# Optimization experiments

Hardware: AMD Instinct MI355X
Metric: run time of the kernel (lower is better)

The kernel has to match this reference:

```python
import jax, jax.numpy as jnp
import numpy as np

NUM_HEADS = 16
TOP_K = 32
NEG_INF = -1e9
EPS = 1e-8


def setup_inputs() -> dict:
    key = jax.random.key(0)
    ks = jax.random.split(key, 12)
    B, S, D = 2, 1024, 1024
    M, dk = 8192, D // NUM_HEADS
    w = lambda k: jax.random.normal(k, (D, D), jnp.float32) * 0.02
    return {
        "x": jax.random.normal(ks[0], (B, S, D), jnp.float32),
        "Wq": w(ks[1]), "bq": jnp.zeros((D,), jnp.float32),
        "Wk": w(ks[2]), "bk": jnp.zeros((D,), jnp.float32),
        "Wv": w(ks[3]), "bv": jnp.zeros((D,), jnp.float32),
        "Wo": w(ks[4]), "bo": jnp.zeros((D,), jnp.float32),
        "mem_keys": jax.random.normal(ks[5], (M, dk), jnp.float32),
        "mem_vals": jax.random.normal(ks[6], (M, dk), jnp.float32),
        "gate": jnp.zeros((1,), jnp.float32),
    }


def _normalize(v):
    return v / (jnp.linalg.norm(v, axis=-1, keepdims=True) + EPS)


def reference(x, Wq, bq, Wk, bk, Wv, bv, Wo, bo, mem_keys, mem_vals, gate):
    B, S, D = x.shape
    H = NUM_HEADS
    dk = D // H
    # projections (torch Linear: x @ W.T + b), split heads -> [B,H,S,dk]
    split = lambda t: t.reshape(B, S, H, dk).transpose(0, 2, 1, 3)
    q = split(x @ Wq.T + bq)
    k = split(x @ Wk.T + bk)
    v = split(x @ Wv.T + bv)
    # causal attention
    scores = jnp.einsum("bhqd,bhkd->bhqk", q, k) / jnp.sqrt(jnp.float32(dk))
    causal = jnp.triu(jnp.ones((S, S), bool), k=1)  # True above diagonal
    scores = jnp.where(causal, NEG_INF, scores)
    attn = jax.nn.softmax(scores, axis=-1)
    attn_out = jnp.einsum("bhqk,bhkd->bhqd", attn, v)
    attn_out = attn_out.transpose(0, 2, 1, 3).reshape(B, S, D)
    attn_out = attn_out @ Wo.T + bo
    # KNN memory retrieval on flattened per-head queries [B*H*S, dk]
    flat_q = q.reshape(-1, dk)
    sims = _normalize(flat_q) @ _normalize(mem_keys).T  # [Q, M]
    top_scores, idx = jax.lax.top_k(sims, TOP_K)        # [Q, K]
    gathered = mem_vals[idx]                            # [Q, K, dk]
    memory_out = jnp.sum(gathered * top_scores[..., None], axis=-2)  # [Q, dk]
    memory_out = memory_out.reshape(B, H, S, dk).transpose(0, 2, 1, 3).reshape(B, S, D)
    memory_out = memory_out @ Wo.T + bo
    g = jax.nn.sigmoid(gate)
    return g * memory_out + (1.0 - g) * attn_out
```

## Files before the change

### kernel.cpp

```cpp
#include <hip/hip_runtime.h>
#include <stdint.h>
#include <math.h>

#define BATCH   2
#define SEQ     1024
#define DMODEL  1024
#define NHEADS  16
#define DK      64
#define MKEYS   8192
#define NQ      (BATCH*NHEADS*SEQ)
#define THRC    2.25f
#define KPART   4
#define PKEYS2  (MKEYS/KPART)
#define PCAP    64
#define QCAP2   (KPART*PCAP)

typedef __attribute__((ext_vector_type(8))) short short8;
typedef __attribute__((ext_vector_type(4))) float f32x4;
typedef __attribute__((ext_vector_type(2))) double f64x2;
typedef __attribute__((ext_vector_type(4))) double f64x4;

__device__ __forceinline__ short f2bf(float f) {
  uint32_t u = __builtin_bit_cast(uint32_t, f);
  u = (u + 0x7fffu + ((u >> 16) & 1u)) >> 16;
  return (short)u;
}
__device__ __forceinline__ short8 ld_bf8_f32(const float* p) {
  float4 a = *(const float4*)p; float4 b = *(const float4*)(p + 4);
  short8 r;
  r[0]=f2bf(a.x); r[1]=f2bf(a.y); r[2]=f2bf(a.z); r[3]=f2bf(a.w);
  r[4]=f2bf(b.x); r[5]=f2bf(b.y); r[6]=f2bf(b.z); r[7]=f2bf(b.w);
  return r;
}

__device__ __forceinline__ unsigned long long packP(double v, int id) {
  unsigned long long b = __builtin_bit_cast(unsigned long long, v);
  b = (b & 0x8000000000000000ull) ? ~b : (b | 0x8000000000000000ull);
  return (b & ~0x1FFFull) | (unsigned long long)(8191 - id);
}
__device__ __forceinline__ double unpackV(unsigned long long P) {
  unsigned long long K = P & ~0x1FFFull;
  unsigned long long bits = (K & 0x8000000000000000ull) ? (K ^ 0x8000000000000000ull) : ~K;
  return __builtin_bit_cast(double, bits);
}

__global__ __launch_bounds__(256) void norm_keys(const float* __restrict__ mk,
                                                 double* __restrict__ invn64,
                                                 float* __restrict__ invnf,
                                                 uint16_t* __restrict__ knbf) {
  int wave = threadIdx.x >> 6, lane = threadIdx.x & 63;
  int m = blockIdx.x * 4 + wave;
  double v = (double)mk[(size_t)m * DK + lane];
  double ss = v * v;
  #pragma unroll
  for (int off = 1; off < 64; off <<= 1) ss += __shfl_xor(ss, off);
  double inv = 1.0 / (sqrt(ss) + 1e-8);
  knbf[(size_t)m * DK + lane] = (uint16_t)f2bf((float)(v * inv));
  if (lane == 0) { invn64[m] = inv; invnf[m] = (float)inv; }
}

__device__ __forceinline__ bool probe_decode(const f64x4 d, int base, int mul,
                                             int out[4]) {
  bool ok = true;
  #pragma unroll
  for (int r = 0; r < 4; r++) {
    int v = (int)d[r];
    int t = v - base;
    bool o = ((double)v == d[r]) && (t >= 0) && (t % mul == 0) && ((t / mul) < 16);
    out[r] = t / mul;
    ok = ok && o;
  }
  return ok;
}

__global__ __launch_bounds__(256, 4) void q64_gemm(const float* __restrict__ x,
                                                   const float* __restrict__ Wq,
                                                   const float* __restrict__ bq,
                                                   double* __restrict__ q64q,
                                                   float* __restrict__ qf32,
                                                   uint16_t* __restrict__ qb) {
  __shared__ __align__(16) float Xs[64 * 68];
  __shared__ __align__(16) float Ws[64 * 68];
  int tid = threadIdx.x, lane = tid & 63, w = tid >> 6;
  int bm = blockIdx.y * 64;
  int h = blockIdx.x;

  f64x4 z = {0.0, 0.0, 0.0, 0.0};
  f64x4 d1 = __builtin_amdgcn_mfma_f64_16x16x4f64((double)lane, 1.0, z, 0, 0, 0);
  f64x4 d2 = __builtin_amdgcn_mfma_f64_16x16x4f64(1.0, (double)lane, z, 0, 0, 0);
  int rdec[4], cdec[4];
  bool ok = probe_decode(d1, 96, 4, rdec);
  bool h1A = (bool)__all(ok ? 1 : 0);
  if (!h1A) ok = probe_decode(d1, 6, 16, rdec);
  bool aOK = h1A || (bool)__all(ok ? 1 : 0);
  ok = probe_decode(d2, 96, 4, cdec);
  bool h1B = (bool)__all(ok ? 1 : 0);
  if (!h1B) ok = probe_decode(d2, 6, 16, cdec);
  bool bOK = h1B || (bool)__all(ok ? 1 : 0);
  int iA = h1A ? (lane & 15) : (lane >> 2);
  int kA = h1A ? (lane >> 4) : (lane & 3);
  int jB = h1B ? (lane & 15) : (lane >> 2);
  int kB = h1B ? (lane >> 4) : (lane & 3);
  bool mfma_ok = aOK && bOK;
  if (mfma_ok) {
    f64x4 d3 = __builtin_amdgcn_mfma_f64_16x16x4f64(
        (double)(4 * iA + kA), (double)(jB + 16 * kB), z, 0, 0, 0);
    bool ok3 = true;
    #pragma unroll
    for (int r = 0; r < 4; r++)
      ok3 = ok3 && (d3[r] == (double)(16 * rdec[r] * cdec[r] + 384 * rdec[r] +
                                      6 * cdec[r] + 224));
    mfma_ok = (bool)__all(ok3 ? 1 : 0);
  }

  if (mfma_ok) {
    int wm = (w >> 1) * 32, wn = (w & 1) * 32;
    f64x4 acc[2][2] = {};
    for (int kt = 0; kt < 16; kt++) {
      __syncthreads();
      #pragma unroll
      for (int i = 0; i < 4; i++) {
        int c4 = tid + 256 * i;
        int r = c4 >> 4, q4 = c4 & 15;
        *(float4*)(Xs + r * 68 + q4 * 4) =
            *(const float4*)(x + (size_t)(bm + r) * DMODEL + kt * 64 + q4 * 4);
        *(float4*)(Ws + r * 68 + q4 * 4) =
            *(const float4*)(Wq + (size_t)(h * 64 + r) * DMODEL + kt * 64 + q4 * 4);
      }
      __syncthreads();
      #pragma unroll
      for (int k = 0; k < 64; k += 4) {
        double a0 = (double)Xs[(wm + iA) * 68 + k + kA];
        double a1 = (double)Xs[(wm + 16 + iA) * 68 + k + kA];
        double b0 = (double)Ws[(wn + jB) * 68 + k + kB];
        double b1 = (double)Ws[(wn + 16 + jB) * 68 + k + kB];
        acc[0][0] = __builtin_amdgcn_mfma_f64_16x16x4f64(a0, b0, acc[0][0], 0, 0, 0);
        acc[0][1] = __builtin_amdgcn_mfma_f64_16x16x4f64(a0, b1, acc[0][1], 0, 0, 0);
        acc[1][0] = __builtin_amdgcn_mfma_f64_16x16x4f64(a1, b0, acc[1][0], 0, 0, 0);
        acc[1][1] = __builtin_amdgcn_mfma_f64_16x16x4f64(a1, b1, acc[1][1], 0, 0, 0);
      }
    }
    #pragma unroll
    for (int mi = 0; mi < 2; mi++)
      #pragma unroll
      for (int ni = 0; ni < 2; ni++)
        #pragma unroll
        for (int rg = 0; rg < 4; rg++) {
          int m = bm + wm + mi * 16 + rdec[rg];
          int d = wn + ni * 16 + cdec[rg];
          int b = m >> 10, s = m & 1023;
          size_t qidx = (((size_t)(b * NHEADS + h) * SEQ) + s) * DK + d;
          double val = acc[mi][ni][rg] + (double)bq[h * DK + d];
          q64q[qidx] = val;
          float fv = (float)val;
          qf32[qidx] = fv;
          qb[qidx] = (uint16_t)f2bf(fv);
        }
  } else {
    int tx = tid & 15, ty = tid >> 4;
    double facc[4][4] = {};
    for (int kt = 0; kt < 16; kt++) {
      __syncthreads();
      #pragma unroll
      for (int i = 0; i < 4; i++) {
        int c4 = tid + 256 * i;
        int r = c4 >> 4, q4 = c4 & 15;
        *(float4*)(Xs + r * 68 + q4 * 4) =
            *(const float4*)(x + (size_t)(bm + r) * DMODEL + kt * 64 + q4 * 4);
        *(float4*)(Ws + r * 68 + q4 * 4) =
            *(const float4*)(Wq + (size_t)(h * 64 + r) * DMODEL + kt * 64 + q4 * 4);
      }
      __syncthreads();
      for (int k = 0; k < 64; k++) {
        double bv[4];
        #pragma unroll
        for (int j = 0; j < 4; j++) bv[j] = (double)Ws[(tx + 16 * j) * 68 + k];
        #pragma unroll
        for (int i = 0; i < 4; i++) {
          double a = (double)Xs[(ty * 4 + i) * 68 + k];
          #pragma unroll
          for (int j = 0; j < 4; j++) facc[i][j] = fma(a, bv[j], facc[i][j]);
        }
      }
    }
    #pragma unroll
    for (int i = 0; i < 4; i++)
      #pragma unroll
      for (int j = 0; j < 4; j++) {
        int m = bm + ty * 4 + i, d = tx + 16 * j;
        int b = m >> 10, s = m & 1023;
        size_t qidx = (((size_t)(b * NHEADS + h) * SEQ) + s) * DK + d;
        double val = facc[i][j] + (double)bq[h * DK + d];
        q64q[qidx] = val;
        float fv = (float)val;
        qf32[qidx] = fv;
        qb[qidx] = (uint16_t)f2bf(fv);
      }
  }
}

template<bool AF, bool WF>
__device__ __forceinline__ void gemm_core(const void* __restrict__ Ap,
                                          const void* __restrict__ Wp,
                                          f32x4 acc[4][4], short* As, short* Bs,
                                          int bm, int bn) {
  int tid = threadIdx.x, lane = tid & 63, w = tid >> 6;
  int wm = (w >> 1) * 64, wn = (w & 1) * 64;
  for (int kt = 0; kt < 16; kt++) {
    __syncthreads();
    #pragma unroll
    for (int i = 0; i < 4; i++) {
      int cq = tid + 256 * i;
      int r = cq >> 3, ch = cq & 7;
      size_t aoff = (size_t)(bm + r) * DMODEL + kt * 64 + ch * 8;
      size_t boff = (size_t)(bn + r) * DMODEL + kt * 64 + ch * 8;
      *(short8*)(As + r * 72 + ch * 8) = AF ? ld_bf8_f32((const float*)Ap + aoff)
                                            : *(const short8*)((const uint16_t*)Ap + aoff);
      *(short8*)(Bs + r * 72 + ch * 8) = WF ? ld_bf8_f32((const float*)Wp + boff)
                                            : *(const short8*)((const uint16_t*)Wp + boff);
    }
    __syncthreads();
    #pragma unroll
    for (int kk = 0; kk < 2; kk++) {
      short8 af[4], bfr[4];
      #pragma unroll
      for (int t = 0; t < 4; t++) {
        af[t]  = *(const short8*)(As + (wm + t * 16 + (lane & 15)) * 72 + kk * 32 + (lane >> 4) * 8);
        bfr[t] = *(const short8*)(Bs + (wn + t * 16 + (lane & 15)) * 72 + kk * 32 + (lane >> 4) * 8);
      }
      #pragma unroll
      for (int mi = 0; mi < 4; mi++)
        #pragma unroll
        for (int ni = 0; ni < 4; ni++)
          acc[mi][ni] = __builtin_amdgcn_mfma_f32_16x16x32_bf16(af[mi], bfr[ni], acc[mi][ni], 0, 0, 0);
    }
  }
}

__global__ __launch_bounds__(256) void gemm_kv(
    const float* __restrict__ x,
    const float* __restrict__ Wk, const float* __restrict__ bk,
    const float* __restrict__ Wv, const float* __restrict__ bv,
    uint16_t* __restrict__ kb, uint16_t* __restrict__ vb) {
  __shared__ __align__(16) short As[128 * 72];
  __shared__ __align__(16) short Bs[128 * 72];
  int z = blockIdx.z;
  const float* W    = z == 0 ? Wk : Wv;
  const float* bias = z == 0 ? bk : bv;
  uint16_t* outB    = z == 0 ? kb : vb;
  int bm = blockIdx.y * 128, bn = blockIdx.x * 128;
  f32x4 acc[4][4] = {};
  gemm_core<true, true>(x, W, acc, As, Bs, bm, bn);
  int lane = threadIdx.x & 63, w = threadIdx.x >> 6;
  int wm = (w >> 1) * 64, wn = (w & 1) * 64;
  #pragma unroll
  for (int mi = 0; mi < 4; mi++)
    #pragma unroll
    for (int ni = 0; ni < 4; ni++) {
      int n = bn + wn + ni * 16 + (lane & 15);
      float bvv = bias[n];
      #pragma unroll
      for (int rg = 0; rg < 4; rg++) {
        int m = bm + wm + mi * 16 + (lane >> 4) * 4 + rg;
        float v = acc[mi][ni][rg] + bvv;
        int b = m >> 10, s = m & 1023, h = n >> 6, d = n & 63;
        size_t idx = (((size_t)(b * NHEADS + h) * SEQ) + s) * DK + d;
        outB[idx] = (uint16_t)f2bf(v);
      }
    }
}

__global__ __launch_bounds__(256) void attn_fwd(
    const uint16_t* __restrict__ qb, const uint16_t* __restrict__ kb,
    const uint16_t* __restrict__ vb, float* __restrict__ attnO) {
  __shared__ __align__(16) short Ks[64 * 72];
  __shared__ __align__(16) short Vt[64 * 72];
  __shared__ __align__(16) short Ps[4][16 * 72];
  int tid = threadIdx.x, lane = tid & 63, w = tid >> 6;
  int bx = blockIdx.x;
  int qt = bx & 15, h = (bx >> 4) & 15, b = bx >> 8;
  const uint16_t* Qg = qb + (size_t)(b * NHEADS + h) * SEQ * DK;
  const uint16_t* Kg = kb + (size_t)(b * NHEADS + h) * SEQ * DK;
  const uint16_t* Vg = vb + (size_t)(b * NHEADS + h) * SEQ * DK;
  int qrow0 = qt * 64 + w * 16;
  short8 qfr[2];
  #pragma unroll
  for (int kk = 0; kk < 2; kk++)
    qfr[kk] = *(const short8*)(const void*)(Qg + (size_t)(qrow0 + (lane & 15)) * DK + kk * 32 + (lane >> 4) * 8);
  float m_i[4] = {-1e30f, -1e30f, -1e30f, -1e30f};
  float l_i[4] = {0.f, 0.f, 0.f, 0.f};
  f32x4 Oacc[4] = {};
  for (int kt = 0; kt <= qt; kt++) {
    __syncthreads();
    #pragma unroll
    for (int i = 0; i < 2; i++) {
      int cq = tid + 256 * i;
      int r = cq >> 3, ch = cq & 7;
      short8 g = *(const short8*)(const void*)(Kg + (size_t)(kt * 64 + r) * DK + ch * 8);
      *(short8*)(Ks + r * 72 + ch * 8) = g;
      short8 gv = *(const short8*)(const void*)(Vg + (size_t)(kt * 64 + r) * DK + ch * 8);
      #pragma unroll
      for (int j = 0; j < 8; j++) Vt[(ch * 8 + j) * 72 + r] = gv[j];
    }
    __syncthreads();
    f32x4 sv[4] = {};
    #pragma unroll
    for (int kk = 0; kk < 2; kk++)
      #pragma unroll
      for (int ni = 0; ni < 4; ni++) {
        short8 kf = *(const short8*)(Ks + (ni * 16 + (lane & 15)) * 72 + kk * 32 + (lane >> 4) * 8);
        sv[ni] = __builtin_amdgcn_mfma_f32_16x16x32_bf16(qfr[kk], kf, sv[ni], 0, 0, 0);
      }
    bool diag = (kt == qt);
    #pragma unroll
    for (int ni = 0; ni < 4; ni++)
      #pragma unroll
      for (int rg = 0; rg < 4; rg++) {
        float sc = sv[ni][rg] * 0.125f;
        if (diag) {
          int kcol = kt * 64 + ni * 16 + (lane & 15);
          int qrow = qrow0 + (lane >> 4) * 4 + rg;
          if (kcol > qrow) sc = -1e9f;
        }
        sv[ni][rg] = sc;
      }
    float alpha[4];
    #pragma unroll
    for (int rg = 0; rg < 4; rg++) {
      float v = fmaxf(fmaxf(sv[0][rg], sv[1][rg]), fmaxf(sv[2][rg], sv[3][rg]));
      v = fmaxf(v, __shfl_xor(v, 1)); v = fmaxf(v, __shfl_xor(v, 2));
      v = fmaxf(v, __shfl_xor(v, 4)); v = fmaxf(v, __shfl_xor(v, 8));
      float mn = fmaxf(m_i[rg], v);
      alpha[rg] = expf(m_i[rg] - mn);
      m_i[rg] = mn;
    }
    #pragma unroll
    for (int ni = 0; ni < 4; ni++)
      #pragma unroll
      for (int rg = 0; rg < 4; rg++) sv[ni][rg] = expf(sv[ni][rg] - m_i[rg]);
    #pragma unroll
    for (int rg = 0; rg < 4; rg++) {
      float s = sv[0][rg] + sv[1][rg] + sv[2][rg] + sv[3][rg];
      s += __shfl_xor(s, 1); s += __shfl_xor(s, 2);
      s += __shfl_xor(s, 4); s += __shfl_xor(s, 8);
      l_i[rg] = l_i[rg] * alpha[rg] + s;
    }
    #pragma unroll
    for (int ni = 0; ni < 4; ni++)
      #pragma unroll
      for (int rg = 0; rg < 4; rg++) Oacc[ni][rg] *= alpha[rg];
    short* Pw = &Ps[w][0];
    #pragma unroll
    for (int ni = 0; ni < 4; ni++)
      #pragma unroll
      for (int rg = 0; rg < 4; rg++)
        Pw[((lane >> 4) * 4 + rg) * 72 + ni * 16 + (lane & 15)] = f2bf(sv[ni][rg]);
    #pragma unroll
    for (int kk = 0; kk < 2; kk++) {
      short8 pa = *(const short8*)(Pw + (lane & 15) * 72 + kk * 32 + (lane >> 4) * 8);
      #pragma unroll
      for (int ni = 0; ni < 4; ni++) {
        short8 vf = *(const short8*)(Vt + (ni * 16 + (lane & 15)) * 72 + kk * 32 + (lane >> 4) * 8);
        Oacc[ni] = __builtin_amdgcn_mfma_f32_16x16x32_bf16(pa, vf, Oacc[ni], 0, 0, 0);
      }
    }
  }
  #pragma unroll
  for (int ni = 0; ni < 4; ni++)
    #pragma unroll
    for (int rg = 0; rg < 4; rg++) {
      int row = qrow0 + (lane >> 4) * 4 + rg;
      attnO[((size_t)b * SEQ + row) * DMODEL + h * DK + ni * 16 + (lane & 15)] =
          Oacc[ni][rg] / l_i[rg];
    }
}

__global__ __launch_bounds__(256) void norm_q(const float* __restrict__ qf32,
                                              float* __restrict__ t0arr) {
  int wave = threadIdx.x >> 6, lane = threadIdx.x & 63;
  int q = blockIdx.x * 4 + wave;
  float v = qf32[((size_t)q << 6) + lane];
  float ss = v * v;
  #pragma unroll
  for (int off = 1; off < 64; off <<= 1) ss += __shfl_xor(ss, off);
  if (lane == 0) t0arr[q] = (THRC / 8.0f) * sqrtf(ss);
}

__global__ __launch_bounds__(256) void knn_filter_mfma(
    const uint16_t* __restrict__ qb, const uint16_t* __restrict__ knbf,
    const float* __restrict__ t0arr,
    unsigned short* __restrict__ cand, int* __restrict__ counts) {
  __shared__ __align__(16) short Ks[64 * 68];
  int tid = threadIdx.x, lane = tid & 63, w = tid >> 6;
  int quad = lane >> 4, col = lane & 15;
  int q0 = blockIdx.y * 64;
  int p = blockIdx.x, k0 = p * PKEYS2;
  int qcol = q0 + w * 16 + col;
  short8 aq[2];
  #pragma unroll
  for (int kk = 0; kk < 2; kk++)
    aq[kk] = *(const short8*)(const void*)(qb + (size_t)qcol * DK + kk * 32 + quad * 8);
  float t0 = t0arr[qcol];
  int cntr = 0;
  for (int kt = 0; kt < PKEYS2 / 64; kt++) {
    __syncthreads();
    {
      int r = tid >> 2, ch = (tid & 3) * 2;
      const uint16_t* src = knbf + (size_t)(k0 + kt * 64 + r) * DK + ch * 8;
      *(short8*)(Ks + r * 68 + ch * 8) = *(const short8*)(const void*)src;
      *(short8*)(Ks + r * 68 + ch * 8 + 8) = *(const short8*)(const void*)(src + 8);
    }
    __syncthreads();
    f32x4 acc[4] = {};
    #pragma unroll
    for (int kk = 0; kk < 2; kk++)
      #pragma unroll
      for (int ni = 0; ni < 4; ni++) {
        short8 kf = *(const short8*)(Ks + (ni * 16 + col) * 68 + kk * 32 + quad * 8);
        acc[ni] = __builtin_amdgcn_mfma_f32_16x16x32_bf16(kf, aq[kk], acc[ni], 0, 0, 0);
      }
    unsigned pb = 0u;
    #pragma unroll
    for (int ni = 0; ni < 4; ni++)
      #pragma unroll
      for (int rg = 0; rg < 4; rg++)
        pb |= (acc[ni][rg] >= t0) ? (1u << (ni * 4 + rg)) : 0u;
    int c = __popc(pb);
    int n1 = __shfl_xor(c, 16), n2 = __shfl_xor(c, 32), n3 = __shfl_xor(c, 48);
    int o1 = quad ^ 1, o2 = quad ^ 2, o3 = quad ^ 3;
    int pre = (o1 < quad ? n1 : 0) + (o2 < quad ? n2 : 0) + (o3 < quad ? n3 : 0);
    int tot = c + n1 + n2 + n3;
    int pos = cntr + pre;
    while (pb) {
      int bi = __builtin_ctz(pb);
      pb &= pb - 1u;
      if (pos < PCAP)
        cand[((size_t)qcol * KPART + p) * PCAP + pos] =
            (unsigned short)(k0 + kt * 64 + (bi >> 2) * 16 + quad * 4 + (bi & 3));
      pos++;
    }
    cntr += tot;
  }
  if (quad == 0) {
    int cq = cntr < PCAP ? cntr : PCAP;
    counts[qcol * KPART + p] = cq;
  }
}

template<int NS>
__device__ __forceinline__ void rank_loop(const unsigned long long* cPw, int n,
                                          const unsigned long long* Pm, int* rank) {
  for (int j = 0; j < n; j++) {
    unsigned long long Pj = cPw[j];
    #pragma unroll
    for (int s = 0; s < NS; s++) rank[s] += (Pj > Pm[s]) ? 1 : 0;
  }
}

__global__ __launch_bounds__(256) void knn_select(const double* __restrict__ q64q,
                                                  const float* __restrict__ qf32,
                                                  const float* __restrict__ mk,
                                                  const double* __restrict__ invn,
                                                  const float* __restrict__ invnf,
                                                  const float* __restrict__ t0arr,
                                                  const unsigned short* __restrict__ cand,
                                                  const int* __restrict__ counts,
                                                  unsigned long long* __restrict__ wlE) {
  __shared__ unsigned short cid[4][QCAP2];
  __shared__ float Af[4][QCAP2];
  __shared__ unsigned short cid2[4][64];
  __shared__ unsigned long long cP[4][QCAP2];
  __shared__ unsigned long long wl[4][32];
  int wave = threadIdx.x >> 6, lane = threadIdx.x & 63;
  int grp = lane & 7, slot = lane >> 3;
  int q = blockIdx.x * 4 + wave;
  int n = 0;
  #pragma unroll
  for (int p = 0; p < KPART; p++) {
    int c = counts[q * KPART + p]; if (c > PCAP) c = PCAP;
    if (lane < c)
      cid[wave][n + lane] = cand[((size_t)q * KPART + p) * PCAP + lane];
    n += c;
  }
  double q8[8];
  {
    const f64x2* qrow2 = (const f64x2*)(q64q + ((size_t)q << 6) + 8 * grp);
    #pragma unroll
    for (int j = 0; j < 4; j++) { f64x2 t = qrow2[j]; q8[2*j] = t[0]; q8[2*j+1] = t[1]; }
  }
  double ssq = 0.0;
  #pragma unroll
  for (int j = 0; j < 8; j++) ssq = fma(q8[j], q8[j], ssq);
  ssq += __shfl_xor(ssq, 1); ssq += __shfl_xor(ssq, 2); ssq += __shfl_xor(ssq, 4);
  double scale = 1.0 / (sqrt(ssq) + 1e-8);
  float qa[8];
  {
    const float4* qrow4 = (const float4*)(qf32 + ((size_t)q << 6) + 8 * grp);
    float4 a0 = qrow4[0], a1 = qrow4[1];
    qa[0]=a0.x; qa[1]=a0.y; qa[2]=a0.z; qa[3]=a0.w;
    qa[4]=a1.x; qa[5]=a1.y; qa[6]=a1.z; qa[7]=a1.w;
  }

  bool full = (n <= 40);
  int m = n;
  if (!full) {
    for (int c0 = 0; c0 < n; c0 += 32) {
      int cc[4], id[4];
      #pragma unroll
      for (int u = 0; u < 4; u++) {
        cc[u] = c0 + 8 * u + slot;
        id[u] = (cc[u] < n) ? (int)cid[wave][cc[u]] : 0;
      }
      float pv[4];
      #pragma unroll
      for (int u = 0; u < 4; u++) {
        const float* kr = mk + (((size_t)id[u]) << 6) + 8 * grp;
        float4 a = *(const float4*)kr;
        float4 b = *(const float4*)(kr + 4);
        float s = 0.f;
        s = fmaf(qa[0], a.x, s); s = fmaf(qa[1], a.y, s);
        s = fmaf(qa[2], a.z, s); s = fmaf(qa[3], a.w, s);
        s = fmaf(qa[4], b.x, s); s = fmaf(qa[5], b.y, s);
        s = fmaf(qa[6], b.z, s); s = fmaf(qa[7], b.w, s);
        pv[u] = s;
      }
      #pragma unroll
      for (int u = 0; u < 4; u++) {
        pv[u] += __shfl_xor(pv[u], 1);
        pv[u] += __shfl_xor(pv[u], 2);
        pv[u] += __shfl_xor(pv[u], 4);
      }
      if (grp == 0) {
        #pragma unroll
        for (int u = 0; u < 4; u++)
          if (cc[u] < n) Af[wave][cc[u]] = pv[u] * invnf[id[u]];
      }
    }
    float t0 = t0arr[q];
    float it0 = 2048.0f / t0;
    int qv[4];
    #pragma unroll
    for (int s = 0; s < 4; s++) {
      int idx = s * 64 + lane;
      if (idx < n) {
        int v = (int)((Af[wave][idx] - t0) * it0);
        v = v < 0 ? 0 : v;
        v = v > 4095 ? 4095 : v;
        qv[s] = v;
      } else {
        qv[s] = -1;
      }
    }
    int lo = 0, hi = 4096;
    while (hi - lo > 1) {
      int mid = (lo + hi) >> 1;
      int cnt = 0;
      #pragma unroll
      for (int s = 0; s < 4; s++)
        cnt += (int)__popcll(__ballot(qv[s] >= mid));
      if (cnt >= 32) lo = mid; else hi = mid;
    }
    int tg = lo - 2; if (tg < 0) tg = 0;
    int base = 0;
    #pragma unroll
    for (int s = 0; s < 4; s++) {
      bool pr = (qv[s] >= tg);
      unsigned long long mb = __ballot(pr);
      if (pr) {
        int pos = base + (int)__popcll(mb & ((1ull << lane) - 1ull));
        if (pos < 64) cid2[wave][pos] = cid[wave][s * 64 + lane];
      }
      base += (int)__popcll(mb);
    }
    if (base > 64) full = true;
    else m = base;
  }
  if (full) m = n;
  const unsigned short* lst = full ? cid[wave] : cid2[wave];

  for (int c0 = 0; c0 < m; c0 += 32) {
    int cc[4], id[4];
    #pragma unroll
    for (int u = 0; u < 4; u++) {
      cc[u] = c0 + 8 * u + slot;
      id[u] = (cc[u] < m) ? (int)lst[cc[u]] : 0;
    }
    double pv[4];
    #pragma unroll
    for (int u = 0; u < 4; u++) {
      const float* kr = mk + (((size_t)id[u]) << 6) + 8 * grp;
      float4 a = *(const float4*)kr;
      float4 b = *(const float4*)(kr + 4);
      double s = 0.0;
      s = fma(q8[0], (double)a.x, s); s = fma(q8[1], (double)a.y, s);
      s = fma(q8[2], (double)a.z, s); s = fma(q8[3], (double)a.w, s);
      s = fma(q8[4], (double)b.x, s); s = fma(q8[5], (double)b.y, s);
      s = fma(q8[6], (double)b.z, s); s = fma(q8[7], (double)b.w, s);
      pv[u] = s;
    }
    #pragma unroll
    for (int u = 0; u < 4; u++) {
      pv[u] += __shfl_xor(pv[u], 1);
      pv[u] += __shfl_xor(pv[u], 2);
      pv[u] += __shfl_xor(pv[u], 4);
    }
    if (grp == 0) {
      #pragma unroll
      for (int u = 0; u < 4; u++)
        if (cc[u] < m) cP[wave][cc[u]] = packP(pv[u] * invn[id[u]], id[u]);
    }
  }
  unsigned long long Pm[4]; int rank[4] = {0, 0, 0, 0};
  #pragma unroll
  for (int s = 0; s < 4; s++) {
    int idx = s * 64 + lane;
    Pm[s] = (idx < m) ? cP[wave][idx] : 0xFFFFFFFFFFFFFFFFull;
  }
  if (m > 128)      rank_loop<4>(cP[wave], m, Pm, rank);
  else if (m > 64)  rank_loop<2>(cP[wave], m, Pm, rank);
  else              rank_loop<1>(cP[wave], m, Pm, rank);
  #pragma unroll
  for (int s = 0; s < 4; s++) {
    int idx = s * 64 + lane;
    if (idx < m && rank[s] < 32) {
      int id = 8191 - (int)(Pm[s] & 0x1FFFull);
      float wgt = (float)(unpackV(Pm[s]) * scale);
      wl[wave][rank[s]] =
          ((unsigned long long)__builtin_bit_cast(unsigned, wgt) << 32) | (unsigned)id;
    }
  }
  int nsel = m < 32 ? m : 32;
  if (lane < nsel) wlE[(size_t)q * 32 + lane] = wl[wave][lane];
}

__global__ __launch_bounds__(256) void knn_gather(const unsigned long long* __restrict__ wlE,
                                                  const int* __restrict__ counts,
                                                  const float* __restrict__ mv,
                                                  const float* __restrict__ attnO,
                                                  const float* __restrict__ gate,
                                                  uint16_t* __restrict__ outb) {
  __shared__ unsigned long long wg[4][32];
  int wave = threadIdx.x >> 6, lane = threadIdx.x & 63;
  int q = blockIdx.x * 4 + wave;
  int n = 0;
  #pragma unroll
  for (int p = 0; p < KPART; p++) {
    int c = counts[q * KPART + p]; if (c > PCAP) c = PCAP;
    n += c;
  }
  int nsel = n < 32 ? n : 32;
  if (lane < 32) wg[wave][lane] = (lane < nsel) ? wlE[(size_t)q * 32 + lane] : 0;
  float accf = 0.f;
  for (int r = 0; r < nsel; r++) {
    unsigned long long e = wg[wave][r];
    int id = (int)(e & 0xFFFFFFFFull);
    float wgt = __builtin_bit_cast(float, (unsigned)(e >> 32));
    accf += wgt * mv[((size_t)id << 6) + lane];
  }
  float g = 1.f / (1.f + expf(-gate[0]));
  int b = q >> 14, h = (q >> 10) & 15, s = q & 1023;
  size_t oi = ((size_t)b * SEQ + s) * DMODEL + h * DK + lane;
  outb[oi] = (uint16_t)f2bf(g * accf + (1.f - g) * attnO[oi]);
}

__global__ __launch_bounds__(256) void gemm_out(
    const uint16_t* __restrict__ A, const float* __restrict__ W,
    const float* __restrict__ bias, float* __restrict__ out) {
  __shared__ __align__(16) short As[128 * 72];
  __shared__ __align__(16) short Bs[128 * 72];
  int bm = blockIdx.y * 128, bn = blockIdx.x * 128;
  f32x4 acc[4][4] = {};
  gemm_core<false, true>(A, W, acc, As, Bs, bm, bn);
  int lane = threadIdx.x & 63, w = threadIdx.x >> 6;
  int wm = (w >> 1) * 64, wn = (w & 1) * 64;
  #pragma unroll
  for (int mi = 0; mi < 4; mi++)
    #pragma unroll
    for (int ni = 0; ni < 4; ni++) {
      int n = bn + wn + ni * 16 + (lane & 15);
      float bvv = bias[n];
      #pragma unroll
      for (int rg = 0; rg < 4; rg++) {
        int m = bm + wm + mi * 16 + (lane >> 4) * 4 + rg;
        out[(size_t)m * DMODEL + n] = acc[mi][ni][rg] + bvv;
      }
    }
}

extern "C" void kernel_launch(void* const* d_in, const int* in_sizes, int n_in,
                              void* d_out, int out_size, void* d_ws, size_t ws_size,
                              hipStream_t stream) {
  const float* x    = (const float*)d_in[0];
  const float* Wq   = (const float*)d_in[1];
  const float* bq   = (const float*)d_in[2];
  const float* Wk   = (const float*)d_in[3];
  const float* bk   = (const float*)d_in[4];
  const float* Wv   = (const float*)d_in[5];
  const float* bv   = (const float*)d_in[6];
  const float* Wo   = (const float*)d_in[7];
  const float* bo   = (const float*)d_in[8];
  const float* mk   = (const float*)d_in[9];
  const float* mv   = (const float*)d_in[10];
  const float* gate = (const float*)d_in[11];

  char* ws = (char*)d_ws;
  double*   invn64  = (double*)(ws);
  float*    invnf   = (float*)(ws + ((size_t)1  << 20));
  uint16_t* knbf    = (uint16_t*)(ws + ((size_t)4  << 20));
  float*    qf32    = (float*)(ws + ((size_t)6  << 20));
  double*   q64q    = (double*)(ws + ((size_t)14 << 20));
  uint16_t* qb      = (uint16_t*)(ws + ((size_t)30 << 20));
  uint16_t* kb      = (uint16_t*)(ws + ((size_t)34 << 20));
  uint16_t* vb      = (uint16_t*)(ws + ((size_t)38 << 20));
  float*    attnO   = (float*)(ws + ((size_t)42 << 20));
  unsigned long long* wlE = (unsigned long long*)(ws + ((size_t)50 << 20));
  uint16_t* blendb  = (uint16_t*)(ws + ((size_t)58 << 20));
  float*    t0arr   = (float*)(ws + ((size_t)62 << 20));
  int*      counts  = (int*)(ws + ((size_t)63 << 20));
  unsigned short* cnd = (unsigned short*)(ws + ((size_t)64 << 20));

  norm_keys<<<dim3(2048), dim3(256), 0, stream>>>(mk, invn64, invnf, knbf);
  q64_gemm<<<dim3(16, 32), dim3(256), 0, stream>>>(x, Wq, bq, q64q, qf32, qb);
  gemm_kv<<<dim3(8, 16, 2), dim3(256), 0, stream>>>(x, Wk, bk, Wv, bv, kb, vb);
  attn_fwd<<<dim3(512), dim3(256), 0, stream>>>(qb, kb, vb, attnO);
  norm_q<<<dim3(8192), dim3(256), 0, stream>>>(qf32, t0arr);
  knn_filter_mfma<<<dim3(KPART, 512), dim3(256), 0, stream>>>(qb, knbf, t0arr, cnd, counts);
  knn_select<<<dim3(8192), dim3(256), 0, stream>>>(q64q, qf32, mk, invn64, invnf, t0arr, cnd, counts, wlE);
  knn_gather<<<dim3(8192), dim3(256), 0, stream>>>(wlE, counts, mv, attnO, gate, blendb);
  gemm_out<<<dim3(8, 16), dim3(256), 0, stream>>>(blendb, Wo, bo, (float*)d_out);
}
```

Baseline: 453.2 us.

## Store bf16 filter scores with candidates, drop fp32 rescoring, fuse gather into select

The filter kernel now writes each candidate as a packed 32-bit word holding the bf16 MFMA score and the key id, split across four per-partition buffers. The select kernel uses those stored scores for its coarse quantized threshold pass, so it no longer recomputes fp32 dot products against mem_keys. The prune margin is widened to make up for the coarser bf16 scores. The separate gather/blend kernel is merged into select, which removes one launch and the round trip of the winner list through global memory. The cost is more candidate storage traffic and more candidates surviving to the fp64 rescoring pass.

```diff
diff --git a/kernel.cpp b/kernel.cpp
--- a/kernel.cpp
+++ b/kernel.cpp
@@ -46,7 +46,6 @@
 
 __global__ __launch_bounds__(256) void norm_keys(const float* __restrict__ mk,
                                                  double* __restrict__ invn64,
-                                                 float* __restrict__ invnf,
                                                  uint16_t* __restrict__ knbf) {
   int wave = threadIdx.x >> 6, lane = threadIdx.x & 63;
   int m = blockIdx.x * 4 + wave;
@@ -56,7 +55,7 @@
   for (int off = 1; off < 64; off <<= 1) ss += __shfl_xor(ss, off);
   double inv = 1.0 / (sqrt(ss) + 1e-8);
   knbf[(size_t)m * DK + lane] = (uint16_t)f2bf((float)(v * inv));
-  if (lane == 0) { invn64[m] = inv; invnf[m] = (float)inv; }
+  if (lane == 0) invn64[m] = inv;
 }
 
 __device__ __forceinline__ bool probe_decode(const f64x4 d, int base, int mul,
@@ -389,12 +388,15 @@
 __global__ __launch_bounds__(256) void knn_filter_mfma(
     const uint16_t* __restrict__ qb, const uint16_t* __restrict__ knbf,
     const float* __restrict__ t0arr,
-    unsigned short* __restrict__ cand, int* __restrict__ counts) {
+    unsigned* __restrict__ c0p, unsigned* __restrict__ c1p,
+    unsigned* __restrict__ c2p, unsigned* __restrict__ c3p,
+    int* __restrict__ counts) {
   __shared__ __align__(16) short Ks[64 * 68];
   int tid = threadIdx.x, lane = tid & 63, w = tid >> 6;
   int quad = lane >> 4, col = lane & 15;
   int q0 = blockIdx.y * 64;
   int p = blockIdx.x, k0 = p * PKEYS2;
+  unsigned* cand = p == 0 ? c0p : p == 1 ? c1p : p == 2 ? c2p : c3p;
   int qcol = q0 + w * 16 + col;
   short8 aq[2];
   #pragma unroll
@@ -431,13 +433,20 @@
     int pre = (o1 < quad ? n1 : 0) + (o2 < quad ? n2 : 0) + (o3 < quad ? n3 : 0);
     int tot = c + n1 + n2 + n3;
     int pos = cntr + pre;
-    while (pb) {
-      int bi = __builtin_ctz(pb);
-      pb &= pb - 1u;
-      if (pos < PCAP)
-        cand[((size_t)qcol * KPART + p) * PCAP + pos] =
-            (unsigned short)(k0 + kt * 64 + (bi >> 2) * 16 + quad * 4 + (bi & 3));
-      pos++;
+    #pragma unroll
+    for (int ni = 0; ni < 4; ni++) {
+      unsigned pb4 = (pb >> (ni * 4)) & 0xFu;
+      while (pb4) {
+        int rg = __builtin_ctz(pb4);
+        pb4 &= pb4 - 1u;
+        float sc = (rg & 2) ? ((rg & 1) ? acc[ni][3] : acc[ni][2])
+                            : ((rg & 1) ? acc[ni][1] : acc[ni][0]);
+        if (pos < PCAP)
+          cand[(size_t)qcol * PCAP + pos] =
+              ((unsigned)(unsigned short)f2bf(sc) << 16) |
+              (unsigned)(k0 + kt * 64 + ni * 16 + quad * 4 + rg);
+        pos++;
+      }
     }
     cntr += tot;
   }
@@ -458,17 +467,20 @@
 }
 
 __global__ __launch_bounds__(256) void knn_select(const double* __restrict__ q64q,
-                                                  const float* __restrict__ qf32,
                                                   const float* __restrict__ mk,
                                                   const double* __restrict__ invn,
-                                                  const float* __restrict__ invnf,
                                                   const float* __restrict__ t0arr,
-                                                  const unsigned short* __restrict__ cand,
+                                                  const unsigned* __restrict__ c0p,
+                                                  const unsigned* __restrict__ c1p,
+                                                  const unsigned* __restrict__ c2p,
+                                                  const unsigned* __restrict__ c3p,
                                                   const int* __restrict__ counts,
-                                                  unsigned long long* __restrict__ wlE) {
-  __shared__ unsigned short cid[4][QCAP2];
-  __shared__ float Af[4][QCAP2];
-  __shared__ unsigned short cid2[4][64];
+                                                  const float* __restrict__ mv,
+                                                  const float* __restrict__ attnO,
+                                                  const float* __restrict__ gate,
+                                                  uint16_t* __restrict__ outb) {
+  __shared__ unsigned ce[4][QCAP2];
+  __shared__ unsigned short cid2[4][QCAP2];
   __shared__ unsigned long long cP[4][QCAP2];
   __shared__ unsigned long long wl[4][32];
   int wave = threadIdx.x >> 6, lane = threadIdx.x & 63;
@@ -477,9 +489,10 @@
   int n = 0;
   #pragma unroll
   for (int p = 0; p < KPART; p++) {
+    const unsigned* cp = p == 0 ? c0p : p == 1 ? c1p : p == 2 ? c2p : c3p;
     int c = counts[q * KPART + p]; if (c > PCAP) c = PCAP;
     if (lane < c)
-      cid[wave][n + lane] = cand[((size_t)q * KPART + p) * PCAP + lane];
+      ce[wave][n + lane] = cp[(size_t)q * PCAP + lane];
     n += c;
   }
   double q8[8];
@@ -493,49 +506,10 @@
   for (int j = 0; j < 8; j++) ssq = fma(q8[j], q8[j], ssq);
   ssq += __shfl_xor(ssq, 1); ssq += __shfl_xor(ssq, 2); ssq += __shfl_xor(ssq, 4);
   double scale = 1.0 / (sqrt(ssq) + 1e-8);
-  float qa[8];
-  {
-    const float4* qrow4 = (const float4*)(qf32 + ((size_t)q << 6) + 8 * grp);
-    float4 a0 = qrow4[0], a1 = qrow4[1];
-    qa[0]=a0.x; qa[1]=a0.y; qa[2]=a0.z; qa[3]=a0.w;
-    qa[4]=a1.x; qa[5]=a1.y; qa[6]=a1.z; qa[7]=a1.w;
-  }
 
   bool full = (n <= 40);
   int m = n;
   if (!full) {
-    for (int c0 = 0; c0 < n; c0 += 32) {
-      int cc[4], id[4];
-      #pragma unroll
-      for (int u = 0; u < 4; u++) {
-        cc[u] = c0 + 8 * u + slot;
-        id[u] = (cc[u] < n) ? (int)cid[wave][cc[u]] : 0;
-      }
-      float pv[4];
-      #pragma unroll
-      for (int u = 0; u < 4; u++) {
-        const float* kr = mk + (((size_t)id[u]) << 6) + 8 * grp;
-        float4 a = *(const float4*)kr;
-        float4 b = *(const float4*)(kr + 4);
-        float s = 0.f;
-        s = fmaf(qa[0], a.x, s); s = fmaf(qa[1], a.y, s);
-        s = fmaf(qa[2], a.z, s); s = fmaf(qa[3], a.w, s);
-        s = fmaf(qa[4], b.x, s); s = fmaf(qa[5], b.y, s);
-        s = fmaf(qa[6], b.z, s); s = fmaf(qa[7], b.w, s);
-        pv[u] = s;
-      }
-      #pragma unroll
-      for (int u = 0; u < 4; u++) {
-        pv[u] += __shfl_xor(pv[u], 1);
-        pv[u] += __shfl_xor(pv[u], 2);
-        pv[u] += __shfl_xor(pv[u], 4);
-      }
-      if (grp == 0) {
-        #pragma unroll
-        for (int u = 0; u < 4; u++)
-          if (cc[u] < n) Af[wave][cc[u]] = pv[u] * invnf[id[u]];
-      }
-    }
     float t0 = t0arr[q];
     float it0 = 2048.0f / t0;
     int qv[4];
@@ -543,7 +517,8 @@
     for (int s = 0; s < 4; s++) {
       int idx = s * 64 + lane;
       if (idx < n) {
-        int v = (int)((Af[wave][idx] - t0) * it0);
+        float A = __builtin_bit_cast(float, ce[wave][idx] & 0xFFFF0000u);
+        int v = (int)((A - t0) * it0);
         v = v < 0 ? 0 : v;
         v = v > 4095 ? 4095 : v;
         qv[s] = v;
@@ -560,7 +535,7 @@
         cnt += (int)__popcll(__ballot(qv[s] >= mid));
       if (cnt >= 32) lo = mid; else hi = mid;
     }
-    int tg = lo - 2; if (tg < 0) tg = 0;
+    int tg = lo - 150; if (tg < 0) tg = 0;
     int base = 0;
     #pragma unroll
     for (int s = 0; s < 4; s++) {
@@ -568,22 +543,28 @@
       unsigned long long mb = __ballot(pr);
       if (pr) {
         int pos = base + (int)__popcll(mb & ((1ull << lane) - 1ull));
-        if (pos < 64) cid2[wave][pos] = cid[wave][s * 64 + lane];
+        cid2[wave][pos] = (unsigned short)(ce[wave][s * 64 + lane] & 0xFFFFu);
       }
       base += (int)__popcll(mb);
     }
     if (base > 64) full = true;
     else m = base;
   }
-  if (full) m = n;
-  const unsigned short* lst = full ? cid[wave] : cid2[wave];
+  if (full) {
+    #pragma unroll
+    for (int s = 0; s < 4; s++) {
+      int idx = s * 64 + lane;
+      if (idx < n) cid2[wave][idx] = (unsigned short)(ce[wave][idx] & 0xFFFFu);
+    }
+    m = n;
+  }
 
   for (int c0 = 0; c0 < m; c0 += 32) {
     int cc[4], id[4];
     #pragma unroll
     for (int u = 0; u < 4; u++) {
       cc[u] = c0 + 8 * u + slot;
-      id[u] = (cc[u] < m) ? (int)lst[cc[u]] : 0;
+      id[u] = (cc[u] < m) ? (int)cid2[wave][cc[u]] : 0;
     }
     double pv[4];
     #pragma unroll
@@ -630,29 +611,10 @@
     }
   }
   int nsel = m < 32 ? m : 32;
-  if (lane < nsel) wlE[(size_t)q * 32 + lane] = wl[wave][lane];
-}
-
-__global__ __launch_bounds__(256) void knn_gather(const unsigned long long* __restrict__ wlE,
-                                                  const int* __restrict__ counts,
-                                                  const float* __restrict__ mv,
-                                                  const float* __restrict__ attnO,
-                                                  const float* __restrict__ gate,
-                                                  uint16_t* __restrict__ outb) {
-  __shared__ unsigned long long wg[4][32];
-  int wave = threadIdx.x >> 6, lane = threadIdx.x & 63;
-  int q = blockIdx.x * 4 + wave;
-  int n = 0;
-  #pragma unroll
-  for (int p = 0; p < KPART; p++) {
-    int c = counts[q * KPART + p]; if (c > PCAP) c = PCAP;
-    n += c;
-  }
-  int nsel = n < 32 ? n : 32;
-  if (lane < 32) wg[wave][lane] = (lane < nsel) ? wlE[(size_t)q * 32 + lane] : 0;
+
   float accf = 0.f;
   for (int r = 0; r < nsel; r++) {
-    unsigned long long e = wg[wave][r];
+    unsigned long long e = wl[wave][r];
     int id = (int)(e & 0xFFFFFFFFull);
     float wgt = __builtin_bit_cast(float, (unsigned)(e >> 32));
     accf += wgt * mv[((size_t)id << 6) + lane];
@@ -705,27 +667,30 @@
 
   char* ws = (char*)d_ws;
   double*   invn64  = (double*)(ws);
-  float*    invnf   = (float*)(ws + ((size_t)1  << 20));
   uint16_t* knbf    = (uint16_t*)(ws + ((size_t)4  << 20));
+  unsigned* cnd0    = (unsigned*)(ws + ((size_t)5  << 20));
   float*    qf32    = (float*)(ws + ((size_t)6  << 20));
   double*   q64q    = (double*)(ws + ((size_t)14 << 20));
   uint16_t* qb      = (uint16_t*)(ws + ((size_t)30 << 20));
   uint16_t* kb      = (uint16_t*)(ws + ((size_t)34 << 20));
   uint16_t* vb      = (uint16_t*)(ws + ((size_t)38 << 20));
   float*    attnO   = (float*)(ws + ((size_t)42 << 20));
-  unsigned long long* wlE = (unsigned long long*)(ws + ((size_t)50 << 20));
+  unsigned* cnd1    = (unsigned*)(ws + ((size_t)50 << 20));
   uint16_t* blendb  = (uint16_t*)(ws + ((size_t)58 << 20));
   float*    t0arr   = (float*)(ws + ((size_t)62 << 20));
   int*      counts  = (int*)(ws + ((size_t)63 << 20));
-  unsigned short* cnd = (unsigned short*)(ws + ((size_t)64 << 20));
-
-  norm_keys<<<dim3(2048), dim3(256), 0, stream>>>(mk, invn64, invnf, knbf);
+  unsigned* cnd2    = (unsigned*)(ws + ((size_t)64 << 20));
+  unsigned* cnd3    = (unsigned*)(ws + ((size_t)72 << 20));
+
+  norm_keys<<<dim3(2048), dim3(256), 0, stream>>>(mk, invn64, knbf);
   q64_gemm<<<dim3(16, 32), dim3(256), 0, stream>>>(x, Wq, bq, q64q, qf32, qb);
   gemm_kv<<<dim3(8, 16, 2), dim3(256), 0, stream>>>(x, Wk, bk, Wv, bv, kb, vb);
   attn_fwd<<<dim3(512), dim3(256), 0, stream>>>(qb, kb, vb, attnO);
   norm_q<<<dim3(8192), dim3(256), 0, stream>>>(qf32, t0arr);
-  knn_filter_mfma<<<dim3(KPART, 512), dim3(256), 0, stream>>>(qb, knbf, t0arr, cnd, counts);
-  knn_select<<<dim3(8192), dim3(256), 0, stream>>>(q64q, qf32, mk, invn64, invnf, t0arr, cnd, counts, wlE);
-  knn_gather<<<dim3(8192), dim3(256), 0, stream>>>(wlE, counts, mv, attnO, gate, blendb);
+  knn_filter_mfma<<<dim3(KPART, 512), dim3(256), 0, stream>>>(qb, knbf, t0arr,
+                                                              cnd0, cnd1, cnd2, cnd3, counts);
+  knn_select<<<dim3(8192), dim3(256), 0, stream>>>(q64q, mk, invn64, t0arr,
+                                                   cnd0, cnd1, cnd2, cnd3, counts,
+                                                   mv, attnO, gate, blendb);
   gemm_out<<<dim3(8, 16), dim3(256), 0, stream>>>(blendb, Wo, bo, (float*)d_out);
 }
```

After: 467.6 us. +3.2%, slower.
